# Kernel tuning notes

Hardware: AMD Instinct MI355X
Metric: run time of the kernel (lower is better)

The kernel has to match this reference:

```python
import jax, jax.numpy as jnp
import numpy as np

B = 1024          # batch
X = 32 * 32       # x_neuron_num
Y = 16384         # y_neuron_num (codebook size)
Z = 1000          # z_neuron_num (classes)
P_BU = 0.5        # y_bottom_up_percent


def _l2n(a, axis):
    # F.normalize: x / max(||x||, 1e-12)
    return a / jnp.maximum(jnp.linalg.norm(a, axis=axis, keepdims=True), 1e-12)


def setup_inputs() -> dict:
    key = jax.random.key(0)
    ks = jax.random.split(key, 8)
    return {
        "x": jax.random.normal(ks[0], (B, 32, 32), jnp.float32),
        "z": jax.random.randint(ks[1], (B,), 0, Z),
        "x2y_w": jax.random.uniform(ks[2], (Y, X), jnp.float32),
        "z2y_w": jax.random.uniform(ks[3], (Y, Z), jnp.float32),
        "y2z_w": jax.random.uniform(ks[4], (Z, Y), jnp.float32),
        "y_age": jax.random.randint(ks[5], (1, Y), 0, 5).astype(jnp.float32),
        "z_age": jax.random.randint(ks[6], (1, Z), 0, 5).astype(jnp.float32),
        "y_threshold": jax.random.uniform(ks[7], (1, Y), jnp.float32) * 0.5,
        "per_item": 1,
    }


def reference(x, z, x2y_w, z2y_w, y2z_w, y_age, z_age, y_threshold, per_item):
    # one 'train' step (torch forward returns inside the per_item loop)
    batch = x.shape[0]
    x = _l2n(x.reshape(batch, -1), 1)                 # [B, X]
    z_hot = jax.nn.one_hot(z, Z, dtype=x.dtype)       # normalized one-hot == one-hot
    Wx = _l2n(x2y_w, 1)                               # [Y, X]
    Wz = _l2n(z2y_w, 1)                               # [Y, Z]
    U = _l2n(y2z_w, 1)                                # [Z, Y]

    y_pre = P_BU * (x @ Wx.T) + (1.0 - P_BU) * (z_hot @ Wz.T)  # [B, Y]

    age = y_age[0]
    thr = y_threshold[0]
    max_resp = jnp.max(y_pre, axis=1)                 # [B]
    max_idx = jnp.argmax(y_pre, axis=1)               # [B]
    # age/threshold tie-break: losers re-argmax over unactivated neurons
    judge = (max_resp > thr[max_idx]) | (age[max_idx] < 1.0)
    unact = (age < 1.0).astype(y_pre.dtype)           # [Y]
    any_unact = jnp.sum(unact) > 0
    fallback = jnp.argmax(y_pre * unact[None, :], axis=1)
    max_idx = jnp.where(judge | ~any_unact, max_idx, fallback)

    # --- Hebbian update of x2y / z2y, expressed as segment reductions ---
    # torch dense form: sum_b y_lr[b,j]*(inp[b]-W[j]) / divisor_j
    ones_b = jnp.ones((batch,), x.dtype)
    cnt = jax.ops.segment_sum(ones_b, max_idx, num_segments=Y)       # [Y]
    div = jnp.where(cnt > 0, cnt, 1.0)
    lr = 1.0 / (age + 1.0)                                           # [Y]
    sumx = jax.ops.segment_sum(x, max_idx, num_segments=Y)           # [Y, X]
    Wx_new = Wx + (lr[:, None] * (sumx - cnt[:, None] * Wx)) / div[:, None]
    sumz = jax.ops.segment_sum(z_hot, max_idx, num_segments=Y)       # [Y, Z]
    Wz_new = Wz + (lr[:, None] * (sumz - cnt[:, None] * Wz)) / div[:, None]
    age_new = age + cnt

    # --- threshold update: per-winner min response (3 for non-winners) ---
    seg_min = jax.ops.segment_min(max_resp, max_idx, num_segments=Y)
    y_cur = jnp.minimum(seg_min, 3.0)
    y_cur = jnp.where(y_cur > 2.0, 0.0, y_cur)
    y_lr_eff = jnp.where(cnt > 0, lr, 0.0)   # sum_b y_lr[b,j]/divisor_j
    thr_new = y_lr_eff * y_cur + (1.0 - y_lr_eff) * thr

    # --- y2z update, segmented by label z ---
    zage = z_age[0]
    zlr = 1.0 / (zage + 1.0)                                          # [Z]
    y_resp = jax.nn.one_hot(max_idx, Y, dtype=x.dtype)                # [B, Y]
    cz = jax.ops.segment_sum(ones_b, z, num_segments=Z)               # [Z]
    dz = jnp.where(cz > 0, cz, 1.0)
    sumy = jax.ops.segment_sum(y_resp, z, num_segments=Z)             # [Z, Y]
    U_new = U + (zlr[:, None] * (sumy - cz[:, None] * U)) / dz[:, None]
    zage_new = zage + cz

    y_activated_num = jnp.sum((age_new >= 1.0).astype(jnp.int32))
    return (y_activated_num, max_resp, Wx_new, Wz_new, U_new,
            thr_new[None, :], age_new[None, :], zage_new[None, :])
```

## Files before the change

### kernel.cpp

```cpp
#include <hip/hip_runtime.h>

#define B_N 1024
#define X_N 1024
#define Y_N 16384
#define Z_N 1000
#define KD  1024
#define MARGIN 0.004f

#define OFF_ACT      0
#define OFF_MAXRESP  1
#define OFF_WX       1025
#define OFF_WZ       16778241
#define OFF_U        33162241
#define OFF_THR      49546241
#define OFF_AGE      49562625
#define OFF_ZAGE     49579009

#define SCR_B_BYTES    4112ull
#define SCR_S_BYTES    67112976ull
#define SCR_A_BYTES    132648976ull
#define SCR_WZT_BYTES  136843280ull

#define WS_INV_X    0
#define WS_INV_WX   1024
#define WS_INV_WZ   17408
#define WS_FIDX     38912
#define WS_CNT      39936
#define WS_ZCNT     56320
#define WS_SEGMIN   57344
#define WS_CTR      73728
#define WS_MBITS    73736

typedef unsigned short ushort_t;
typedef _Float16 f16x8 __attribute__((ext_vector_type(8)));
typedef float f32x4 __attribute__((ext_vector_type(4)));

__device__ __forceinline__ unsigned enc_f(float f) {
    unsigned u = __float_as_uint(f);
    return (u & 0x80000000u) ? ~u : (u | 0x80000000u);
}
__device__ __forceinline__ float dec_f(unsigned e) {
    unsigned u = (e & 0x80000000u) ? (e ^ 0x80000000u) : ~e;
    return __uint_as_float(u);
}
__device__ __forceinline__ unsigned long long pack_vi(float v, int y) {
    return ((unsigned long long)enc_f(v) << 32) |
           (unsigned long long)(0xFFFFFFFFu - (unsigned)y);
}
__device__ __forceinline__ ushort_t f2h(float f) {
    _Float16 h = (_Float16)f;
    ushort_t u; __builtin_memcpy(&u, &h, 2); return u;
}
__device__ __forceinline__ float h2f(unsigned lo16) {
    ushort_t u = (ushort_t)lo16; _Float16 h;
    __builtin_memcpy(&h, &u, 2); return (float)h;
}

#define GLOAD16(gp, lp) __builtin_amdgcn_global_load_lds( \
    (const __attribute__((address_space(1))) void*)(gp),  \
    (__attribute__((address_space(3))) void*)(lp), 16, 0, 0)

__global__ void init_kernel(int* cnt, unsigned* segmin, int* zcnt, int* ctr) {
    int i = blockIdx.x * 256 + threadIdx.x;
    if (i < Y_N) { cnt[i] = 0; segmin[i] = 0xFFFFFFFFu; }
    if (i < 1024) zcnt[i] = 0;
    if (i < 8) ctr[i] = (i == 2) ? 0x7FFFFFFF : 0;
}

__global__ __launch_bounds__(256) void prep_kernel(
    const float* __restrict__ y_age, int* ctr, unsigned long long* __restrict__ mbits,
    const float* __restrict__ x, ushort_t* __restrict__ A, float* __restrict__ inv_x,
    const float* __restrict__ wxw, const float* __restrict__ wzw,
    ushort_t* __restrict__ Bm, float* __restrict__ inv_wx, float* __restrict__ inv_wz) {
    const int bid = blockIdx.x, t = threadIdx.x;
    const int lane = t & 63, wid = t >> 6;
    __shared__ float red1[4], red2[4];

    if (bid < 64) {
        int i = bid * 256 + t;
        int a = (y_age[i] < 1.0f) ? 1 : 0;
        unsigned long long m = __ballot(a);
        int mi = a ? 0x7FFFFFFF : i;
        #pragma unroll
        for (int s = 32; s > 0; s >>= 1) mi = min(mi, __shfl_xor(mi, s, 64));
        if (lane == 0) {
            atomicAdd(ctr, (int)__popcll(m));
            mbits[i >> 6] = m;
            if (mi != 0x7FFFFFFF) atomicMin(&ctr[2], mi);
        }
    } else if (bid < 64 + B_N) {
        int b = bid - 64;
        float4 v = reinterpret_cast<const float4*>(x + (size_t)b * X_N)[t];
        float ss = v.x*v.x + v.y*v.y + v.z*v.z + v.w*v.w;
        #pragma unroll
        for (int s = 32; s > 0; s >>= 1) ss += __shfl_xor(ss, s, 64);
        if (lane == 0) red1[wid] = ss;
        __syncthreads();
        float inv = 1.0f / fmaxf(sqrtf(red1[0] + red1[1] + red1[2] + red1[3]), 1e-12f);
        if (t == 0) inv_x[b] = inv;
        ushort_t o1[4] = { f2h(v.x*inv), f2h(v.y*inv), f2h(v.z*inv), f2h(v.w*inv) };
        *reinterpret_cast<uint2*>(A + (size_t)b * KD + t * 4) = *reinterpret_cast<uint2*>(o1);
    } else {
        int y = bid - 64 - B_N;
        float4 a = reinterpret_cast<const float4*>(wxw + (size_t)y * X_N)[t];
        float4 zv = make_float4(0.f, 0.f, 0.f, 0.f);
        if (t < 250) zv = reinterpret_cast<const float4*>(wzw + (size_t)y * Z_N)[t];
        float s1 = a.x*a.x + a.y*a.y + a.z*a.z + a.w*a.w;
        float s2 = zv.x*zv.x + zv.y*zv.y + zv.z*zv.z + zv.w*zv.w;
        #pragma unroll
        for (int s = 32; s > 0; s >>= 1) {
            s1 += __shfl_xor(s1, s, 64);
            s2 += __shfl_xor(s2, s, 64);
        }
        if (lane == 0) { red1[wid] = s1; red2[wid] = s2; }
        __syncthreads();
        float inv1 = 1.0f / fmaxf(sqrtf(red1[0] + red1[1] + red1[2] + red1[3]), 1e-12f);
        float inv2 = 1.0f / fmaxf(sqrtf(red2[0] + red2[1] + red2[2] + red2[3]), 1e-12f);
        ushort_t o1[4] = { f2h(a.x*inv1), f2h(a.y*inv1), f2h(a.z*inv1), f2h(a.w*inv1) };
        *reinterpret_cast<uint2*>(Bm + (size_t)y * KD + t * 4) = *reinterpret_cast<uint2*>(o1);
        if (t == 0) { inv_wx[y] = inv1; inv_wz[y] = inv2; }
    }
}

__global__ __launch_bounds__(256) void wzt_kernel(
    const float* __restrict__ wzw, const float* __restrict__ inv_wz,
    ushort_t* __restrict__ wzt) {
    const int bid = blockIdx.x;
    const int z0 = (bid & 15) * 64, y0 = (bid >> 4) * 64;
    const int t = threadIdx.x;
    __shared__ float tile[64][65];
    #pragma unroll
    for (int p = 0; p < 4; ++p) {
        int yr = p * 16 + (t >> 4);
        int z = z0 + (t & 15) * 4;
        float4 v = make_float4(0.f, 0.f, 0.f, 0.f);
        if (z + 3 < Z_N)
            v = *reinterpret_cast<const float4*>(wzw + (size_t)(y0 + yr) * Z_N + z);
        float s = 0.5f * inv_wz[y0 + yr];
        tile[(t & 15) * 4 + 0][yr] = v.x * s;
        tile[(t & 15) * 4 + 1][yr] = v.y * s;
        tile[(t & 15) * 4 + 2][yr] = v.z * s;
        tile[(t & 15) * 4 + 3][yr] = v.w * s;
    }
    __syncthreads();
    #pragma unroll
    for (int p = 0; p < 4; ++p) {
        int zr = p * 16 + (t >> 4);
        int yc = (t & 15) * 4;
        if (z0 + zr < 1024) {
            ushort_t o[4] = { f2h(tile[zr][yc]), f2h(tile[zr][yc + 1]),
                              f2h(tile[zr][yc + 2]), f2h(tile[zr][yc + 3]) };
            *reinterpret_cast<uint2*>(wzt + (size_t)(z0 + zr) * Y_N + y0 + yc) =
                *reinterpret_cast<uint2*>(o);
        }
    }
}

__global__ __launch_bounds__(512, 1) void mm256_kernel(const ushort_t* __restrict__ A,
                                                       const ushort_t* __restrict__ Bm,
                                                       ushort_t* __restrict__ S) {
    __shared__ __align__(16) _Float16 lds[4][2][1024][8];
    const int t = threadIdx.x;
    const int wid = t >> 6, lane = t & 63;
    const int bid = blockIdx.x;
    const int lb = (bid & 7) * 32 + (bid >> 3);
    const int mt = lb & 3, nt = lb >> 2;
    const int b0 = mt * 256, y0 = nt * 256;
    const int wr = wid >> 2, wc = wid & 3;
    const int r = lane & 15, gq = lane >> 4;
    const int NK = KD / 32;

    f32x4 acc[8][4];
    #pragma unroll
    for (int i = 0; i < 8; ++i)
        #pragma unroll
        for (int j = 0; j < 4; ++j) acc[i][j] = (f32x4){0.f, 0.f, 0.f, 0.f};

    auto stage = [&](int buf, int k0) {
        #pragma unroll
        for (int rr = 0; rr < 2; ++rr) {
            int s = rr * 512 + t;
            int row = s & 255, g = s >> 8;
            GLOAD16(A  + (size_t)(b0 + row) * KD + k0 + g * 8, &lds[buf][0][s][0]);
            GLOAD16(Bm + (size_t)(y0 + row) * KD + k0 + g * 8, &lds[buf][1][s][0]);
        }
    };

    stage(0, 0);
    stage(1, 32);
    stage(2, 64);
    asm volatile("s_waitcnt vmcnt(8)" ::: "memory");
    __builtin_amdgcn_s_barrier();
    asm volatile("" ::: "memory");

    for (int ks = 0; ks < NK; ++ks) {
        const int cur = ks & 3;
        f16x8 bF[4];
        #pragma unroll
        for (int nf = 0; nf < 4; ++nf)
            bF[nf] = *reinterpret_cast<const f16x8*>(
                &lds[cur][1][gq * 256 + wc * 64 + nf * 16 + r][0]);
        __builtin_amdgcn_s_setprio(1);
        #pragma unroll
        for (int mf = 0; mf < 8; ++mf) {
            f16x8 aF = *reinterpret_cast<const f16x8*>(
                &lds[cur][0][gq * 256 + wr * 128 + mf * 16 + r][0]);
            #pragma unroll
            for (int nf = 0; nf < 4; ++nf)
                acc[mf][nf] = __builtin_amdgcn_mfma_f32_16x16x32_f16(
                    aF, bF[nf], acc[mf][nf], 0, 0, 0);
        }
        __builtin_amdgcn_s_setprio(0);
        if (ks == NK - 1) break;

        __builtin_amdgcn_s_barrier();
        asm volatile("" ::: "memory");
        if (ks + 3 < NK) {
            stage((ks + 3) & 3, (ks + 3) * 32);
            asm volatile("s_waitcnt vmcnt(8)" ::: "memory");
        } else if (ks + 3 == NK) {
            asm volatile("s_waitcnt vmcnt(4)" ::: "memory");
        } else {
            asm volatile("s_waitcnt vmcnt(0)" ::: "memory");
        }
        __builtin_amdgcn_s_barrier();
        asm volatile("" ::: "memory");
    }

    #pragma unroll
    for (int mf = 0; mf < 8; ++mf) {
        int bg = b0 + wr * 128 + mf * 16 + gq * 4;
        #pragma unroll
        for (int nf = 0; nf < 4; ++nf) {
            int yg = y0 + wc * 64 + nf * 16 + r;
            f32x4 c = acc[mf][nf];
            #pragma unroll
            for (int q = 0; q < 4; ++q)
                S[(size_t)(bg + q) * Y_N + yg] = f2h(0.5f * c[q]);
        }
    }
}

__global__ __launch_bounds__(256) void scanres_kernel(
    const ushort_t* __restrict__ scores, const ushort_t* __restrict__ wzt,
    const int* __restrict__ zlab, const unsigned long long* __restrict__ mbits,
    const int* __restrict__ ctr,
    const float* __restrict__ x, const float* __restrict__ inv_x,
    const float* __restrict__ wxw, const float* __restrict__ inv_wx,
    const float* __restrict__ wzw, const float* __restrict__ inv_wz,
    const float* __restrict__ y_thr, const float* __restrict__ y_age,
    int* final_idx, int* cnt, unsigned* segmin, int* zcnt,
    float* __restrict__ out_maxresp) {
    const int b = blockIdx.x, t = threadIdx.x;
    const int lane = t & 63, wid = t >> 6;
    const int zb = zlab[b];
    const uint4* srow = reinterpret_cast<const uint4*>(scores + (size_t)b * Y_N);
    const uint4* wrow = reinterpret_cast<const uint4*>(wzt + (size_t)zb * Y_N);

    __shared__ float rv[4], rm[4];
    __shared__ int nA_s, nB_s;
    __shared__ int cA[256], cB[256];
    __shared__ unsigned long long red[4];
    __shared__ unsigned long long sPM;
    __shared__ int sTakeA;

    float vmax = -1e30f, mmax = -1e30f;
    for (int c = t; c < Y_N / 8; c += 256) {
        uint4 pk = srow[c];
        uint4 wz = wrow[c];
        int yb = c * 8;
        unsigned m8 = (unsigned)((mbits[yb >> 6] >> (yb & 63)) & 0xFFull);
        unsigned w[4] = {pk.x, pk.y, pk.z, pk.w};
        unsigned q[4] = {wz.x, wz.y, wz.z, wz.w};
        #pragma unroll
        for (int j = 0; j < 4; ++j) {
            float v0 = h2f(w[j] & 0xFFFFu) + h2f(q[j] & 0xFFFFu);
            float v1 = h2f(w[j] >> 16) + h2f(q[j] >> 16);
            vmax = fmaxf(vmax, fmaxf(v0, v1));
            mmax = fmaxf(mmax, v0 * (float)((m8 >> (2 * j)) & 1u));
            mmax = fmaxf(mmax, v1 * (float)((m8 >> (2 * j + 1)) & 1u));
        }
    }
    #pragma unroll
    for (int s = 32; s > 0; s >>= 1) {
        vmax = fmaxf(vmax, __shfl_xor(vmax, s, 64));
        mmax = fmaxf(mmax, __shfl_xor(mmax, s, 64));
    }
    if (lane == 0) { rv[wid] = vmax; rm[wid] = mmax; }
    if (t == 0) { nA_s = 0; nB_s = 0; }
    __syncthreads();
    float tA = fmaxf(fmaxf(rv[0], rv[1]), fmaxf(rv[2], rv[3])) - MARGIN;
    float tB = fmaxf(fmaxf(rm[0], rm[1]), fmaxf(rm[2], rm[3])) - MARGIN;
    bool anyu = ctr[0] > 0;

    for (int c = t; c < Y_N / 8; c += 256) {
        uint4 pk = srow[c];
        uint4 wz = wrow[c];
        int yb = c * 8;
        unsigned m8 = (unsigned)((mbits[yb >> 6] >> (yb & 63)) & 0xFFull);
        unsigned w[4] = {pk.x, pk.y, pk.z, pk.w};
        unsigned q[4] = {wz.x, wz.y, wz.z, wz.w};
        #pragma unroll
        for (int j = 0; j < 8; ++j) {
            unsigned sw = (j & 1) ? (w[j >> 1] >> 16) : (w[j >> 1] & 0xFFFFu);
            unsigned qw = (j & 1) ? (q[j >> 1] >> 16) : (q[j >> 1] & 0xFFFFu);
            float v = h2f(sw) + h2f(qw);
            if (v >= tA) { int p = atomicAdd(&nA_s, 1); if (p < 256) cA[p] = yb + j; }
            if (anyu && ((m8 >> j) & 1u) && v >= tB) {
                int p = atomicAdd(&nB_s, 1); if (p < 256) cB[p] = yb + j;
            }
        }
    }
    __syncthreads();
    int nA = min(nA_s, 256), nB = min(nB_s, 256);

    float invx = inv_x[b];
    const float4* xr = reinterpret_cast<const float4*>(x + (size_t)b * X_N);
    float4 xv[4];
    #pragma unroll
    for (int j = 0; j < 4; ++j) xv[j] = xr[j * 64 + lane];

    unsigned long long bA = 0ull;
    for (int c = wid; c < nA; c += 8) {
        int y1 = cA[c];
        int c2 = c + 4;
        bool h2 = c2 < nA;
        int y2 = cA[h2 ? c2 : c];
        const float4* w1 = reinterpret_cast<const float4*>(wxw + (size_t)y1 * X_N);
        const float4* w2 = reinterpret_cast<const float4*>(wxw + (size_t)y2 * X_N);
        float d1 = 0.f, d2 = 0.f;
        #pragma unroll
        for (int j = 0; j < 4; ++j) {
            float4 a1 = w1[j * 64 + lane];
            float4 a2 = w2[j * 64 + lane];
            d1 += xv[j].x*a1.x + xv[j].y*a1.y + xv[j].z*a1.z + xv[j].w*a1.w;
            d2 += xv[j].x*a2.x + xv[j].y*a2.y + xv[j].z*a2.z + xv[j].w*a2.w;
        }
        #pragma unroll
        for (int s = 32; s > 0; s >>= 1) {
            d1 += __shfl_xor(d1, s, 64);
            d2 += __shfl_xor(d2, s, 64);
        }
        float v1 = 0.5f*invx*inv_wx[y1]*d1 + 0.5f*inv_wz[y1]*wzw[(size_t)y1*Z_N + zb];
        unsigned long long p1 = pack_vi(v1, y1);
        bA = (p1 > bA) ? p1 : bA;
        if (h2) {
            float v2 = 0.5f*invx*inv_wx[y2]*d2 + 0.5f*inv_wz[y2]*wzw[(size_t)y2*Z_N + zb];
            unsigned long long p2 = pack_vi(v2, y2);
            bA = (p2 > bA) ? p2 : bA;
        }
    }
    if (lane == 0) red[wid] = bA;
    __syncthreads();
    if (t == 0) {
        unsigned long long pm = red[0];
        #pragma unroll
        for (int j = 1; j < 4; ++j) pm = (red[j] > pm) ? red[j] : pm;
        sPM = pm;
        unsigned enc = (unsigned)(pm >> 32);
        int idx = (int)(0xFFFFFFFFu - (unsigned)(pm & 0xFFFFFFFFull));
        float mresp = dec_f(enc);
        out_maxresp[b] = mresp;
        bool judge = (mresp > y_thr[idx]) || (y_age[idx] < 1.0f);
        sTakeA = (judge || !anyu) ? 1 : 0;
    }
    __syncthreads();

    if (!sTakeA) {
        unsigned long long bB = 0ull;
        for (int c = wid; c < nB; c += 8) {
            int y1 = cB[c];
            int c2 = c + 4;
            bool h2 = c2 < nB;
            int y2 = cB[h2 ? c2 : c];
            const float4* w1 = reinterpret_cast<const float4*>(wxw + (size_t)y1 * X_N);
            const float4* w2 = reinterpret_cast<const float4*>(wxw + (size_t)y2 * X_N);
            float d1 = 0.f, d2 = 0.f;
            #pragma unroll
            for (int j = 0; j < 4; ++j) {
                float4 a1 = w1[j * 64 + lane];
                float4 a2 = w2[j * 64 + lane];
                d1 += xv[j].x*a1.x + xv[j].y*a1.y + xv[j].z*a1.z + xv[j].w*a1.w;
                d2 += xv[j].x*a2.x + xv[j].y*a2.y + xv[j].z*a2.z + xv[j].w*a2.w;
            }
            #pragma unroll
            for (int s = 32; s > 0; s >>= 1) {
                d1 += __shfl_xor(d1, s, 64);
                d2 += __shfl_xor(d2, s, 64);
            }
            float v1 = 0.5f*invx*inv_wx[y1]*d1 + 0.5f*inv_wz[y1]*wzw[(size_t)y1*Z_N + zb];
            unsigned long long p1 = pack_vi(v1, y1);
            bB = (p1 > bB) ? p1 : bB;
            if (h2) {
                float v2 = 0.5f*invx*inv_wx[y2]*d2 + 0.5f*inv_wz[y2]*wzw[(size_t)y2*Z_N + zb];
                unsigned long long p2 = pack_vi(v2, y2);
                bB = (p2 > bB) ? p2 : bB;
            }
        }
        if (lane == 0) red[wid] = bB;
    }
    __syncthreads();
    if (t == 0) {
        unsigned long long pm = sPM;
        unsigned enc = (unsigned)(pm >> 32);
        int idx = (int)(0xFFFFFFFFu - (unsigned)(pm & 0xFFFFFFFFull));
        int fin;
        if (sTakeA) {
            fin = idx;
        } else if (nB > 0) {
            unsigned long long pf = red[0];
            #pragma unroll
            for (int j = 1; j < 4; ++j) pf = (red[j] > pf) ? red[j] : pf;
            fin = (int)(0xFFFFFFFFu - (unsigned)(pf & 0xFFFFFFFFull));
        } else {
            fin = ctr[2];
        }
        final_idx[b] = fin;
        atomicAdd(&cnt[fin], 1);
        atomicMin(&segmin[fin], enc);
        atomicAdd(&zcnt[zb], 1);
    }
}

__global__ __launch_bounds__(256) void out_kernel(
    const float* __restrict__ wxw, const float* __restrict__ inv_wx,
    const float* __restrict__ x, const float* __restrict__ inv_x,
    const float* __restrict__ wzw, const float* __restrict__ inv_wz,
    const float* __restrict__ uw, const int* __restrict__ zlab,
    const int* __restrict__ final_idx, const int* __restrict__ cnt,
    const int* __restrict__ zcnt, const unsigned* __restrict__ segmin,
    const float* __restrict__ y_age, const float* __restrict__ z_age,
    const float* __restrict__ y_thr, float* __restrict__ out, int* ctr) {
    const int bid = blockIdx.x, t = threadIdx.x;
    const int lane = t & 63, wid = t >> 6;
    __shared__ int s_idx[1024];
    __shared__ int s_n;
    __shared__ float rss[4];

    if (bid < Z_N) {
        int cz = bid;
        if (t == 0) s_n = 0;
        const float4* rowp4 = reinterpret_cast<const float4*>(uw + (size_t)cz * Y_N);
        float4 u[16];
        float ss = 0.f;
        #pragma unroll
        for (int p = 0; p < 16; ++p) {
            u[p] = rowp4[p * 256 + t];
            ss += u[p].x*u[p].x + u[p].y*u[p].y + u[p].z*u[p].z + u[p].w*u[p].w;
        }
        #pragma unroll
        for (int s = 32; s > 0; s >>= 1) ss += __shfl_xor(ss, s, 64);
        if (lane == 0) rss[wid] = ss;
        __syncthreads();
        float inv = 1.0f / fmaxf(sqrtf(rss[0] + rss[1] + rss[2] + rss[3]), 1e-12f);
        int c = zcnt[cz];
        if (c > 0) {
            for (int b = t; b < B_N; b += 256)
                if (zlab[b] == cz) { int p = atomicAdd(&s_n, 1); s_idx[p] = final_idx[b]; }
        }
        __syncthreads();
        float zlr = 1.0f / (z_age[cz] + 1.0f);
        float fc = (float)c;
        float dv = (c > 0) ? fc : 1.0f;
        float f = zlr / dv;
        int n = s_n;
        float* outp = out + OFF_U + (size_t)cz * Y_N;
        #pragma unroll
        for (int p = 0; p < 16; ++p) {
            int e4 = p * 256 + t;
            float4 un = make_float4(u[p].x*inv, u[p].y*inv, u[p].z*inv, u[p].w*inv);
            if (c > 0) {
                float4 s = make_float4(0.f, 0.f, 0.f, 0.f);
                for (int m = 0; m < n; ++m) {
                    int d = s_idx[m] - e4 * 4;
                    if (d == 0) s.x += 1.f;
                    else if (d == 1) s.y += 1.f;
                    else if (d == 2) s.z += 1.f;
                    else if (d == 3) s.w += 1.f;
                }
                un.x += f * (s.x - fc * un.x);
                un.y += f * (s.y - fc * un.y);
                un.z += f * (s.z - fc * un.z);
                un.w += f * (s.w - fc * un.w);
            }
            *reinterpret_cast<float4*>(outp + e4 * 4) = un;
        }
    } else if (bid < Z_N + Y_N) {
        int j = bid - Z_N;
        if (t == 0) s_n = 0;
        __syncthreads();
        int c = cnt[j];
        if (c > 0) {
            for (int b = t; b < B_N; b += 256)
                if (final_idx[b] == j) { int p = atomicAdd(&s_n, 1); s_idx[p] = b; }
        }
        __syncthreads();
        float inv = inv_wx[j];
        float lr = 1.0f / (y_age[j] + 1.0f);
        float fc = (float)c;
        float dv = (c > 0) ? fc : 1.0f;
        int n = s_n;
        float4 w = *reinterpret_cast<const float4*>(wxw + (size_t)j * X_N + t * 4);
        float4 wn = make_float4(w.x*inv, w.y*inv, w.z*inv, w.w*inv);
        if (c > 0) {
            float4 s = make_float4(0.f, 0.f, 0.f, 0.f);
            for (int m = 0; m < n; ++m) {
                int b = s_idx[m];
                float ix = inv_x[b];
                float4 xv = *reinterpret_cast<const float4*>(x + (size_t)b * X_N + t * 4);
                s.x += xv.x * ix; s.y += xv.y * ix; s.z += xv.z * ix; s.w += xv.w * ix;
            }
            float f = lr / dv;
            wn.x += f * (s.x - fc * wn.x);
            wn.y += f * (s.y - fc * wn.y);
            wn.z += f * (s.z - fc * wn.z);
            wn.w += f * (s.w - fc * wn.w);
        }
        *reinterpret_cast<float4*>(out + OFF_WX + (size_t)j * X_N + t * 4) = wn;
    } else if (bid < Z_N + 2 * Y_N) {
        int j = bid - Z_N - Y_N;
        if (t == 0) s_n = 0;
        __syncthreads();
        int c = cnt[j];
        if (c > 0) {
            for (int b = t; b < B_N; b += 256)
                if (final_idx[b] == j) { int p = atomicAdd(&s_n, 1); s_idx[p] = zlab[b]; }
        }
        __syncthreads();
        if (t >= 250) return;
        float inv = inv_wz[j];
        float lr = 1.0f / (y_age[j] + 1.0f);
        float fc = (float)c;
        float dv = (c > 0) ? fc : 1.0f;
        int n = s_n;
        float4 w = *reinterpret_cast<const float4*>(wzw + (size_t)j * Z_N + t * 4);
        float4 wn = make_float4(w.x*inv, w.y*inv, w.z*inv, w.w*inv);
        if (c > 0) {
            float4 s = make_float4(0.f, 0.f, 0.f, 0.f);
            for (int m = 0; m < n; ++m) {
                int d = s_idx[m] - t * 4;
                if (d == 0) s.x += 1.f;
                else if (d == 1) s.y += 1.f;
                else if (d == 2) s.z += 1.f;
                else if (d == 3) s.w += 1.f;
            }
            float f = lr / dv;
            wn.x += f * (s.x - fc * wn.x);
            wn.y += f * (s.y - fc * wn.y);
            wn.z += f * (s.z - fc * wn.z);
            wn.w += f * (s.w - fc * wn.w);
        }
        *reinterpret_cast<float4*>(out + OFF_WZ + (size_t)j * Z_N + t * 4) = wn;
    } else if (bid < Z_N + 2 * Y_N + 64) {
        int j = (bid - Z_N - 2 * Y_N) * 256 + t;
        int c = cnt[j];
        float age = y_age[j];
        float thr = y_thr[j];
        float tn = thr;
        if (c > 0) {
            float lr = 1.0f / (age + 1.0f);
            float smin = dec_f(segmin[j]);
            float ycur = fminf(smin, 3.0f);
            if (ycur > 2.0f) ycur = 0.0f;
            tn = lr * ycur + (1.0f - lr) * thr;
        }
        out[OFF_THR + j] = tn;
        float an = age + (float)c;
        out[OFF_AGE + j] = an;
        unsigned long long m = __ballot(an >= 1.0f ? 1 : 0);
        if (lane == 0) atomicAdd(ctr + 1, (int)__popcll(m));
    } else {
        int i = (bid - Z_N - 2 * Y_N - 64) * 256 + t;
        if (i < Z_N) out[OFF_ZAGE + i] = z_age[i] + (float)zcnt[i];
    }
}

__global__ void act_kernel(const int* __restrict__ ctr, float* __restrict__ out_act) {
    if (threadIdx.x == 0) out_act[0] = (float)ctr[1];
}

extern "C" void kernel_launch(void* const* d_in, const int* in_sizes, int n_in,
                              void* d_out, int out_size, void* d_ws, size_t ws_size,
                              hipStream_t stream) {
    const float* x     = (const float*)d_in[0];
    const int*   z     = (const int*)d_in[1];
    const float* wxw   = (const float*)d_in[2];
    const float* wzw   = (const float*)d_in[3];
    const float* uw    = (const float*)d_in[4];
    const float* y_age = (const float*)d_in[5];
    const float* z_age = (const float*)d_in[6];
    const float* y_thr = (const float*)d_in[7];
    float* out = (float*)d_out;
    float* ws  = (float*)d_ws;
    char*  ob  = (char*)d_out;

    float* inv_x  = ws + WS_INV_X;
    float* inv_wx = ws + WS_INV_WX;
    float* inv_wz = ws + WS_INV_WZ;
    int* fidx = (int*)(ws + WS_FIDX);
    int* cnt  = (int*)(ws + WS_CNT);
    int* zcnt = (int*)(ws + WS_ZCNT);
    unsigned* segmin = (unsigned*)(ws + WS_SEGMIN);
    int* ctr = (int*)(ws + WS_CTR);
    unsigned long long* mbits = (unsigned long long*)(ws + WS_MBITS);

    ushort_t* Bb  = (ushort_t*)(ob + SCR_B_BYTES);
    ushort_t* Sc  = (ushort_t*)(ob + SCR_S_BYTES);
    ushort_t* Ab  = (ushort_t*)(ob + SCR_A_BYTES);
    ushort_t* wzt = (ushort_t*)(ob + SCR_WZT_BYTES);

    init_kernel<<<64, 256, 0, stream>>>(cnt, segmin, zcnt, ctr);
    prep_kernel<<<64 + B_N + Y_N, 256, 0, stream>>>(y_age, ctr, mbits, x, Ab, inv_x,
                                                    wxw, wzw, Bb, inv_wx, inv_wz);
    wzt_kernel<<<16 * 256, 256, 0, stream>>>(wzw, inv_wz, wzt);
    mm256_kernel<<<(B_N / 256) * (Y_N / 256), 512, 0, stream>>>(Ab, Bb, Sc);
    scanres_kernel<<<B_N, 256, 0, stream>>>(Sc, wzt, z, mbits, ctr, x, inv_x,
                                            wxw, inv_wx, wzw, inv_wz, y_thr, y_age,
                                            fidx, cnt, segmin, zcnt, out + OFF_MAXRESP);
    out_kernel<<<Z_N + 2 * Y_N + 64 + 4, 256, 0, stream>>>(
        wxw, inv_wx, x, inv_x, wzw, inv_wz, uw, z, fidx, cnt, zcnt, segmin,
        y_age, z_age, y_thr, out, ctr);
    act_kernel<<<1, 64, 0, stream>>>(ctr, out + OFF_ACT);
}
```

Measured before the change: 235.8 us.

## Load GEMM A fragments directly from global into registers, stage only B in LDS

The 256x256 GEMM tile now runs with 1024 threads (16 waves, each owning a 64x64 sub-tile). It stages only the B operand in LDS and loads each wave's A fragments straight from global memory into double-buffered registers. This halves the LDS footprint and the LDS read traffic, and adds waves for latency hiding. The cost is that A is read redundantly from global/L2 by the four waves sharing a row band, and the vmcnt accounting becomes more fragile.

```diff
diff --git a/kernel.cpp b/kernel.cpp
--- a/kernel.cpp
+++ b/kernel.cpp
@@ -156,83 +156,103 @@
     }
 }
 
-__global__ __launch_bounds__(512, 1) void mm256_kernel(const ushort_t* __restrict__ A,
-                                                       const ushort_t* __restrict__ Bm,
-                                                       ushort_t* __restrict__ S) {
-    __shared__ __align__(16) _Float16 lds[4][2][1024][8];
+__global__ __launch_bounds__(1024, 3) void mm256_kernel(const ushort_t* __restrict__ A,
+                                                        const ushort_t* __restrict__ Bm,
+                                                        ushort_t* __restrict__ S) {
+    __shared__ __align__(16) _Float16 lds[4][1024][8];
     const int t = threadIdx.x;
     const int wid = t >> 6, lane = t & 63;
     const int bid = blockIdx.x;
     const int lb = (bid & 7) * 32 + (bid >> 3);
     const int mt = lb & 3, nt = lb >> 2;
     const int b0 = mt * 256, y0 = nt * 256;
-    const int wr = wid >> 2, wc = wid & 3;
+    const int wm = wid >> 2, wn = wid & 3;
     const int r = lane & 15, gq = lane >> 4;
     const int NK = KD / 32;
 
-    f32x4 acc[8][4];
+    f32x4 acc[4][4];
     #pragma unroll
-    for (int i = 0; i < 8; ++i)
+    for (int i = 0; i < 4; ++i)
         #pragma unroll
         for (int j = 0; j < 4; ++j) acc[i][j] = (f32x4){0.f, 0.f, 0.f, 0.f};
 
     auto stage = [&](int buf, int k0) {
-        #pragma unroll
-        for (int rr = 0; rr < 2; ++rr) {
-            int s = rr * 512 + t;
-            int row = s & 255, g = s >> 8;
-            GLOAD16(A  + (size_t)(b0 + row) * KD + k0 + g * 8, &lds[buf][0][s][0]);
-            GLOAD16(Bm + (size_t)(y0 + row) * KD + k0 + g * 8, &lds[buf][1][s][0]);
-        }
+        int row = t & 255, g = t >> 8;
+        GLOAD16(Bm + (size_t)(y0 + row) * KD + k0 + g * 8, &lds[buf][g * 256 + row][0]);
     };
-
+    auto loadA = [&](f16x8 (&dst)[4], int ks) {
+        #pragma unroll
+        for (int mf = 0; mf < 4; ++mf)
+            dst[mf] = *reinterpret_cast<const f16x8*>(
+                A + (size_t)(b0 + wm * 64 + mf * 16 + r) * KD + ks * 32 + gq * 8);
+    };
+    auto compute = [&](int cur, f16x8 (&aF)[4]) {
+        f16x8 bF[4];
+        #pragma unroll
+        for (int nf = 0; nf < 4; ++nf)
+            bF[nf] = *reinterpret_cast<const f16x8*>(
+                &lds[cur][gq * 256 + wn * 64 + nf * 16 + r][0]);
+        __builtin_amdgcn_s_setprio(1);
+        #pragma unroll
+        for (int mf = 0; mf < 4; ++mf)
+            #pragma unroll
+            for (int nf = 0; nf < 4; ++nf)
+                acc[mf][nf] = __builtin_amdgcn_mfma_f32_16x16x32_f16(
+                    aF[mf], bF[nf], acc[mf][nf], 0, 0, 0);
+        __builtin_amdgcn_s_setprio(0);
+    };
+
+    f16x8 aA[4], aB[4];
+    loadA(aA, 0);
     stage(0, 0);
     stage(1, 32);
     stage(2, 64);
-    asm volatile("s_waitcnt vmcnt(8)" ::: "memory");
+    asm volatile("s_waitcnt vmcnt(2)" ::: "memory");
     __builtin_amdgcn_s_barrier();
     asm volatile("" ::: "memory");
 
-    for (int ks = 0; ks < NK; ++ks) {
-        const int cur = ks & 3;
-        f16x8 bF[4];
-        #pragma unroll
-        for (int nf = 0; nf < 4; ++nf)
-            bF[nf] = *reinterpret_cast<const f16x8*>(
-                &lds[cur][1][gq * 256 + wc * 64 + nf * 16 + r][0]);
-        __builtin_amdgcn_s_setprio(1);
-        #pragma unroll
-        for (int mf = 0; mf < 8; ++mf) {
-            f16x8 aF = *reinterpret_cast<const f16x8*>(
-                &lds[cur][0][gq * 256 + wr * 128 + mf * 16 + r][0]);
-            #pragma unroll
-            for (int nf = 0; nf < 4; ++nf)
-                acc[mf][nf] = __builtin_amdgcn_mfma_f32_16x16x32_f16(
-                    aF, bF[nf], acc[mf][nf], 0, 0, 0);
-        }
-        __builtin_amdgcn_s_setprio(0);
-        if (ks == NK - 1) break;
-
-        __builtin_amdgcn_s_barrier();
-        asm volatile("" ::: "memory");
-        if (ks + 3 < NK) {
-            stage((ks + 3) & 3, (ks + 3) * 32);
-            asm volatile("s_waitcnt vmcnt(8)" ::: "memory");
-        } else if (ks + 3 == NK) {
-            asm volatile("s_waitcnt vmcnt(4)" ::: "memory");
-        } else {
-            asm volatile("s_waitcnt vmcnt(0)" ::: "memory");
-        }
-        __builtin_amdgcn_s_barrier();
-        asm volatile("" ::: "memory");
+    for (int ks = 0; ks < NK; ks += 2) {
+        if (ks + 1 < NK) loadA(aB, ks + 1);
+        compute(ks & 3, aA);
+        {
+            __builtin_amdgcn_s_barrier();
+            asm volatile("" ::: "memory");
+            if (ks + 3 < NK) {
+                stage((ks + 3) & 3, (ks + 3) * 32);
+                asm volatile("s_waitcnt vmcnt(6)" ::: "memory");
+            } else if (ks + 3 == NK) {
+                asm volatile("s_waitcnt vmcnt(5)" ::: "memory");
+            } else {
+                asm volatile("s_waitcnt vmcnt(4)" ::: "memory");
+            }
+            __builtin_amdgcn_s_barrier();
+            asm volatile("" ::: "memory");
+        }
+        if (ks + 2 < NK) loadA(aA, ks + 2);
+        compute((ks + 1) & 3, aB);
+        if (ks + 1 == NK - 1) break;
+        {
+            __builtin_amdgcn_s_barrier();
+            asm volatile("" ::: "memory");
+            if (ks + 4 < NK) {
+                stage((ks + 4) & 3, (ks + 4) * 32);
+                asm volatile("s_waitcnt vmcnt(6)" ::: "memory");
+            } else if (ks + 4 == NK) {
+                asm volatile("s_waitcnt vmcnt(5)" ::: "memory");
+            } else {
+                asm volatile("s_waitcnt vmcnt(4)" ::: "memory");
+            }
+            __builtin_amdgcn_s_barrier();
+            asm volatile("" ::: "memory");
+        }
     }
 
     #pragma unroll
-    for (int mf = 0; mf < 8; ++mf) {
-        int bg = b0 + wr * 128 + mf * 16 + gq * 4;
+    for (int mf = 0; mf < 4; ++mf) {
+        int bg = b0 + wm * 64 + mf * 16 + gq * 4;
         #pragma unroll
         for (int nf = 0; nf < 4; ++nf) {
-            int yg = y0 + wc * 64 + nf * 16 + r;
+            int yg = y0 + wn * 64 + nf * 16 + r;
             f32x4 c = acc[mf][nf];
             #pragma unroll
             for (int q = 0; q < 4; ++q)
@@ -613,7 +633,7 @@
     prep_kernel<<<64 + B_N + Y_N, 256, 0, stream>>>(y_age, ctr, mbits, x, Ab, inv_x,
                                                     wxw, wzw, Bb, inv_wx, inv_wz);
     wzt_kernel<<<16 * 256, 256, 0, stream>>>(wzw, inv_wz, wzt);
-    mm256_kernel<<<(B_N / 256) * (Y_N / 256), 512, 0, stream>>>(Ab, Bb, Sc);
+    mm256_kernel<<<(B_N / 256) * (Y_N / 256), 1024, 0, stream>>>(Ab, Bb, Sc);
     scanres_kernel<<<B_N, 256, 0, stream>>>(Sc, wzt, z, mbits, ctr, x, inv_x,
                                             wxw, inv_wx, wzw, inv_wz, y_thr, y_age,
                                             fidx, cnt, segmin, zcnt, out + OFF_MAXRESP);
```

Measured after the change: 261.4 us. +10.9%, slower.
